# Performance work log

Measured on AMD Instinct MI355X. Metric: run time of the kernel, lower is better.

## Reference

```python
import jax, jax.numpy as jnp
import numpy as np

D, F, E, K = 1024, 2048, 8, 2
EPS = 1.1920929e-07  # torch.finfo(float32).eps, RMSNorm default eps=None


def setup_inputs() -> dict:
    key = jax.random.key(0)
    ks = jax.random.split(key, 6)
    x = jax.random.normal(ks[0], (2, 2048, D), jnp.float32)
    Wg = jax.random.normal(ks[1], (D, E), jnp.float32)          # Gate.weights ~ randn
    norm_w = jnp.ones((E, D), jnp.float32)                       # per-expert RMSNorm weight
    W1 = jax.random.normal(ks[2], (E, D, F), jnp.float32) * 0.02
    b1 = jnp.zeros((E, F), jnp.float32)
    W2 = jax.random.normal(ks[3], (E, D, F), jnp.float32) * 0.02
    b2 = jnp.zeros((E, F), jnp.float32)
    W3 = jax.random.normal(ks[4], (E, F, D), jnp.float32) * 0.02
    b3 = jnp.zeros((E, D), jnp.float32)
    return {"x": x, "Wg": Wg, "norm_w": norm_w, "W1": W1, "b1": b1,
            "W2": W2, "b2": b2, "W3": W3, "b3": b3, "k": K}


def reference(x, Wg, norm_w, W1, b1, W2, b2, W3, b3, k):
    orig_shape = x.shape
    xt = x.reshape(-1, x.shape[-1])                    # [T, d]
    num_experts = Wg.shape[-1]

    # --- Gate: top-k then softmax over selected logits ---
    scores = xt @ Wg                                   # [T, E]
    top_v, top_i = jax.lax.top_k(scores, k)            # [T, k]
    gates = jax.nn.softmax(top_v, axis=-1)             # [T, k]
    # combine weight per (token, expert); zero for unrouted experts
    comb = jnp.einsum('tk,tke->te', gates,
                      jax.nn.one_hot(top_i, num_experts, dtype=gates.dtype))  # [T, E]

    # --- Per-expert SwiGLU FFN with RMSNorm (norm weight folded into W1/W2) ---
    inv = jax.lax.rsqrt(jnp.mean(xt * xt, axis=-1, keepdims=True) + EPS)
    xh = xt * inv                                      # [T, d] (un-weighted RMSNorm)
    W1p = norm_w[:, :, None] * W1                      # [E, d, f]
    W2p = norm_w[:, :, None] * W2
    a = jnp.einsum('td,edf->etf', xh, W1p) + b1[:, None, :]   # [E, T, f]
    g = jnp.einsum('td,edf->etf', xh, W2p) + b2[:, None, :]
    h = jax.nn.silu(a) * g                             # [E, T, f]
    o = jnp.einsum('etf,efd->etd', h, W3) + b3[:, None, :]    # [E, T, d]

    # --- Weighted combine (comb==0 for unrouted -> identical to masked loop) ---
    y = jnp.einsum('etd,te->td', o, comb)              # [T, d]
    return y.reshape(orig_shape)
```

## Files before the change

### kernel.cpp

```cpp
#include <hip/hip_runtime.h>
#include <hip/hip_bf16.h>

typedef unsigned short u16;
typedef __attribute__((ext_vector_type(8))) short bf16x8;
typedef __attribute__((ext_vector_type(4))) float f32x4;

#define D_DIM 1024
#define F_DIM 2048
#define E_NUM 8
#define EPS_RMS 1.1920929e-07f
#define NCHUNK 16

__device__ __forceinline__ u16 f2bf(float f) {
  union { float f; unsigned u; } v; v.f = f;
  unsigned r = v.u + 0x7FFFu + ((v.u >> 16) & 1u);
  return (u16)(r >> 16);
}

__device__ __forceinline__ void async16(const void* g, void* l) {
  __builtin_amdgcn_global_load_lds((const __attribute__((address_space(1))) void*)g,
                                   (__attribute__((address_space(3))) void*)l, 16, 0, 0);
}

__global__ __launch_bounds__(256) void prep_kernel(
    const float* __restrict__ W1, const float* __restrict__ W2,
    const float* __restrict__ W3, const float* __restrict__ scale,
    const float* __restrict__ x, const float* __restrict__ Wg,
    u16* __restrict__ Wc, u16* __restrict__ W3t, u16* __restrict__ xh,
    int* __restrict__ topi, float* __restrict__ gatev)
{
  __shared__ float tile[128][65];
  __shared__ float red[4][9];
  __shared__ float invs;
  const int lin = blockIdx.x;
  const int tid = threadIdx.x;

  if (lin < 4096) {
    const int z = lin >> 8;
    const int rem = lin & 255;
    const int fb = (rem & 31) * 64;
    const int db = (rem >> 5) * 128;
    const int e = z & 7;
    const float* W = (z < 8) ? W1 : W2;
    const int gofs = (z < 8) ? 0 : 16;
    const float* Wp = W + (size_t)e * D_DIM * F_DIM;
#pragma unroll
    for (int s = 0; s < 8; ++s) {
      const int d = (tid >> 4) + s * 16;
      float4 v = *reinterpret_cast<const float4*>(Wp + (size_t)(db + d) * F_DIM + fb + (tid & 15) * 4);
      tile[d][(tid&15)*4+0] = v.x; tile[d][(tid&15)*4+1] = v.y;
      tile[d][(tid&15)*4+2] = v.z; tile[d][(tid&15)*4+3] = v.w;
    }
    __syncthreads();
    const int dx = (tid & 31) * 4;
    float sc[4];
#pragma unroll
    for (int q = 0; q < 4; ++q) sc[q] = scale[(size_t)e * D_DIM + db + dx + q];
    u16* op = Wc + (size_t)e * (2*F_DIM) * D_DIM;
#pragma unroll
    for (int p = 0; p < 8; ++p) {
      const int j = (tid >> 5) + p * 8;
      const int c = fb + j;
      const int rphys = ((c >> 4) << 5) + (c & 15) + gofs;
      u16 tmp[4];
#pragma unroll
      for (int q = 0; q < 4; ++q) tmp[q] = f2bf(tile[dx + q][j] * sc[q]);
      *reinterpret_cast<ushort4*>(op + (size_t)rphys * D_DIM + db + dx) =
          *reinterpret_cast<ushort4*>(tmp);
    }
  } else if (lin < 6144) {
    const int l2 = lin - 4096;
    const int e = l2 >> 8;
    const int rem = l2 & 255;
    const int dt = (rem & 15) * 64;
    const int ft = (rem >> 4) * 128;
    const float* Wp = W3 + (size_t)e * F_DIM * D_DIM;
#pragma unroll
    for (int s = 0; s < 8; ++s) {
      const int fr = (tid >> 4) + s * 16;
      float4 v = *reinterpret_cast<const float4*>(Wp + (size_t)(ft + fr) * D_DIM + dt + (tid & 15) * 4);
      tile[fr][(tid&15)*4+0] = v.x; tile[fr][(tid&15)*4+1] = v.y;
      tile[fr][(tid&15)*4+2] = v.z; tile[fr][(tid&15)*4+3] = v.w;
    }
    __syncthreads();
    const int fx = (tid & 31) * 4;
    u16* op = W3t + (size_t)e * D_DIM * F_DIM;
#pragma unroll
    for (int p = 0; p < 8; ++p) {
      const int j = (tid >> 5) + p * 8;
      u16 tmp[4];
#pragma unroll
      for (int q = 0; q < 4; ++q) tmp[q] = f2bf(tile[fx + q][j]);
      *reinterpret_cast<ushort4*>(op + (size_t)(dt + j) * F_DIM + ft + fx) =
          *reinterpret_cast<ushort4*>(tmp);
    }
  } else {
    const int t = lin - 6144;
    const float4 xv = reinterpret_cast<const float4*>(x + (size_t)t * D_DIM)[tid];
    float ss = xv.x*xv.x + xv.y*xv.y + xv.z*xv.z + xv.w*xv.w;
    float s[8];
#pragma unroll
    for (int e = 0; e < 8; ++e) s[e] = 0.f;
    const float xa[4] = {xv.x, xv.y, xv.z, xv.w};
#pragma unroll
    for (int j = 0; j < 4; ++j) {
      const float4* wr = reinterpret_cast<const float4*>(Wg + (size_t)(tid*4 + j) * 8);
      float4 w0 = wr[0], w1 = wr[1];
      s[0] += xa[j]*w0.x; s[1] += xa[j]*w0.y; s[2] += xa[j]*w0.z; s[3] += xa[j]*w0.w;
      s[4] += xa[j]*w1.x; s[5] += xa[j]*w1.y; s[6] += xa[j]*w1.z; s[7] += xa[j]*w1.w;
    }
#pragma unroll
    for (int off = 32; off > 0; off >>= 1) {
      ss += __shfl_down(ss, off);
#pragma unroll
      for (int e = 0; e < 8; ++e) s[e] += __shfl_down(s[e], off);
    }
    const int wv = tid >> 6, lane = tid & 63;
    if (lane == 0) { red[wv][8] = ss;
#pragma unroll
      for (int e = 0; e < 8; ++e) red[wv][e] = s[e]; }
    __syncthreads();
    if (tid == 0) {
      float sum2 = red[0][8] + red[1][8] + red[2][8] + red[3][8];
      invs = rsqrtf(sum2 * (1.0f / D_DIM) + EPS_RMS);
      float sc[8];
#pragma unroll
      for (int e = 0; e < 8; ++e) sc[e] = red[0][e] + red[1][e] + red[2][e] + red[3][e];
      int i0 = 0; float v0 = sc[0];
#pragma unroll
      for (int e = 1; e < 8; ++e) if (sc[e] > v0) { v0 = sc[e]; i0 = e; }
      int i1 = -1; float v1 = -3.0e38f;
#pragma unroll
      for (int e = 0; e < 8; ++e) if (e != i0 && sc[e] > v1) { v1 = sc[e]; i1 = e; }
      float p1 = 1.0f / (1.0f + expf(v0 - v1));
      float p0 = 1.0f - p1;
      topi[2*t] = i0; topi[2*t+1] = i1;
      gatev[2*t] = p0; gatev[2*t+1] = p1;
    }
    __syncthreads();
    const float inv = invs;
    ushort4 o;
    o.x = f2bf(xv.x*inv); o.y = f2bf(xv.y*inv); o.z = f2bf(xv.z*inv); o.w = f2bf(xv.w*inv);
    reinterpret_cast<ushort4*>(xh + (size_t)t * D_DIM)[tid] = o;
  }
}

__global__ __launch_bounds__(256) void count_kernel(
    const int* __restrict__ topi, int* __restrict__ percnt, int nent)
{
  const int blk = blockIdx.x;
  const int tid = threadIdx.x;
  const int per = (nent + NCHUNK*256 - 1) / (NCHUNK*256);
  const int cbase = blk * 256 * per;
  int c[8];
#pragma unroll
  for (int q = 0; q < 8; ++q) c[q] = 0;
  for (int i = 0; i < per; ++i) {
    const int idx = cbase + tid * per + i;
    if (idx < nent) {
      const int e = topi[idx];
#pragma unroll
      for (int q = 0; q < 8; ++q) c[q] += (e == q) ? 1 : 0;
    }
  }
#pragma unroll
  for (int off = 32; off > 0; off >>= 1)
#pragma unroll
    for (int q = 0; q < 8; ++q) c[q] += __shfl_down(c[q], off);
  __shared__ int red[4][8];
  const int wv = tid >> 6, lane = tid & 63;
  if (lane == 0)
#pragma unroll
    for (int q = 0; q < 8; ++q) red[wv][q] = c[q];
  __syncthreads();
  if (tid < 8) percnt[blk * 8 + tid] = red[0][tid] + red[1][tid] + red[2][tid] + red[3][tid];
}

__global__ __launch_bounds__(256) void scatter_kernel(
    const int* __restrict__ topi, const int* __restrict__ percnt,
    int* __restrict__ rowtok, int* __restrict__ slots, int* __restrict__ offs, int nent)
{
  __shared__ int cur[8];
  const int blk = blockIdx.x, tid = threadIdx.x;
  if (tid == 0) {
    int tot[8];
#pragma unroll
    for (int e = 0; e < 8; ++e) {
      tot[e] = 0;
      for (int c = 0; c < NCHUNK; ++c) tot[e] += percnt[c*8 + e];
    }
    int acc = 0, start[8];
#pragma unroll
    for (int e = 0; e < 8; ++e) {
      start[e] = acc;
      if (blk == 0) offs[e] = acc;
      acc += (tot[e] + 255) & ~255;
    }
    if (blk == 0) offs[8] = acc;
    for (int c = 0; c < blk; ++c)
#pragma unroll
      for (int e = 0; e < 8; ++e) start[e] += percnt[c*8 + e];
#pragma unroll
    for (int e = 0; e < 8; ++e) cur[e] = start[e];
  }
  __syncthreads();
  const int per = (nent + NCHUNK*256 - 1) / (NCHUNK*256);
  const int cbase = blk * 256 * per;
  for (int i = 0; i < per; ++i) {
    const int idx = cbase + tid * per + i;
    if (idx < nent) {
      const int e = topi[idx];
      const int pos = atomicAdd(&cur[e], 1);
      rowtok[pos] = idx >> 1;
      slots[idx] = pos;
    }
  }
}

__global__ __launch_bounds__(512, 4) void ffn1_kernel(
    const u16* __restrict__ xh, const u16* __restrict__ Wc,
    const float* __restrict__ b1, const float* __restrict__ b2,
    const int* __restrict__ rowtok, const int* __restrict__ offs,
    u16* __restrict__ h)
{
  __shared__ __align__(16) u16 smem[36864];

  const int row0 = blockIdx.y * 256;
  if (row0 >= offs[8]) return;
  int e = 0;
#pragma unroll
  for (int i = 1; i < 8; ++i) e += (row0 >= offs[i]) ? 1 : 0;

  const int bx = blockIdx.x;
  const int n0p = bx * 128;
  const int tid = threadIdx.x;
  const int lane = tid & 63;
  const int l15 = lane & 15;
  const int wv = tid >> 6;
  const int wm = wv >> 1;
  const int wn = wv & 1;

  int arow[2];
  const u16* gAp[2];
#pragma unroll
  for (int j = 0; j < 2; ++j) {
    const int i = tid + 512*j;
    const int p = i >> 3;
    const int v = (i & 7) ^ (p & 7);
    arow[j] = 2*p + (v >> 2);
    int tk = rowtok[row0 + arow[j]];
    if (tk < 0) tk = 0;
    gAp[j] = xh + (size_t)tk * D_DIM + (v & 3) * 8;
  }
  const u16* gBp;
  {
    const int i = tid;
    const int p = i >> 3;
    const int v = (i & 7) ^ (p & 7);
    const int brow = 2*p + (v >> 2);
    gBp = Wc + ((size_t)e * (2*F_DIM) + n0p + brow) * D_DIM + (v & 3) * 8;
  }

  const f32x4 zero = {0.f, 0.f, 0.f, 0.f};
  f32x4 acc[4][4];
#pragma unroll
  for (int i = 0; i < 4; ++i)
#pragma unroll
    for (int j = 0; j < 4; ++j) acc[i][j] = zero;

  const int rlane = (((l15 & 1) << 2) + (lane >> 4)) ^ (l15 >> 1);
  const int aoff = (l15 >> 1) * 64 + rlane * 8;
  const int boff = (l15 >> 1) * 64 + rlane * 8;

#define STAGE1(b, k0)                                                       \
  {                                                                         \
    const int base_ = (b) * 12288;                                          \
    async16(gAp[0] + (k0), &smem[base_ + tid*8]);                           \
    async16(gAp[1] + (k0), &smem[base_ + (tid + 512)*8]);                   \
    async16(gBp   + (k0), &smem[base_ + 8192 + tid*8]);                     \
  }

  STAGE1(0, 0);
  STAGE1(1, 32);

  const int NSTEP = D_DIM / 32;
  for (int t = 0; t < NSTEP; ++t) {
    const int bsel = t % 3;
    if (t + 1 < NSTEP) {
      asm volatile("s_waitcnt vmcnt(3)" ::: "memory");
    } else {
      asm volatile("s_waitcnt vmcnt(0)" ::: "memory");
    }
    __builtin_amdgcn_s_barrier();
    if (t + 2 < NSTEP) {
      const int bn = (t + 2) % 3;
      const int kn = (t + 2) * 32;
      STAGE1(bn, kn);
    }
    const int aB = bsel * 12288, bB = aB + 8192;
    bf16x8 af[4], bv[4];
#pragma unroll
    for (int mi = 0; mi < 4; ++mi)
      af[mi] = *(const bf16x8*)(&smem[aB + (wm*32 + mi*8)*64 + aoff]);
#pragma unroll
    for (int ni = 0; ni < 4; ++ni)
      bv[ni] = *(const bf16x8*)(&smem[bB + (wn*32 + ni*8)*64 + boff]);
#pragma unroll
    for (int mi = 0; mi < 4; ++mi)
#pragma unroll
      for (int ni = 0; ni < 4; ++ni)
        acc[mi][ni] = __builtin_amdgcn_mfma_f32_16x16x32_bf16(af[mi], bv[ni], acc[mi][ni], 0, 0, 0);
  }
#undef STAGE1

#pragma unroll
  for (int mi = 0; mi < 4; ++mi) {
    const int rbase = row0 + wm*64 + mi*16 + (lane >> 4)*4;
#pragma unroll
    for (int q = 0; q < 2; ++q) {
      const int rc = bx*64 + wn*32 + q*16 + l15;
      const float bb1 = b1[e*F_DIM + rc], bb2 = b2[e*F_DIM + rc];
#pragma unroll
      for (int r = 0; r < 4; ++r) {
        float a = acc[mi][2*q][r] + bb1;
        float g = acc[mi][2*q+1][r] + bb2;
        h[(size_t)(rbase + r) * F_DIM + rc] = f2bf(a / (1.f + __expf(-a)) * g);
      }
    }
  }
}

__global__ __launch_bounds__(256, 2) void ffn2_kernel(
    const u16* __restrict__ h, const u16* __restrict__ W3t,
    const float* __restrict__ b3, const int* __restrict__ offs,
    float* __restrict__ opart)
{
  __shared__ __align__(16) u16 smem[32768];

  const int lin = blockIdx.y * gridDim.x + blockIdx.x;
  const int qc  = (gridDim.x * gridDim.y) >> 3;
  const int L   = (lin & 7) * qc + (lin >> 3);
  const int bx  = L % gridDim.x;
  const int by  = L / gridDim.x;

  const int row0 = by * 128;
  if (row0 >= offs[8]) return;
  int e = 0;
#pragma unroll
  for (int i = 1; i < 8; ++i) e += (row0 >= offs[i]) ? 1 : 0;

  const int n0 = bx * 128;
  const int tid = threadIdx.x;
  const int lane = tid & 63;
  const int wv = tid >> 6;
  const int wm = wv >> 1;
  const int wn = wv & 1;

  const int srow = tid >> 3;
  const int sseg = (tid & 7) ^ (srow & 7);
  const u16* gA[4]; const u16* gB[4];
#pragma unroll
  for (int j = 0; j < 4; ++j) {
    gA[j] = h   + (size_t)(row0 + srow + 32*j) * F_DIM + sseg * 8;
    gB[j] = W3t + ((size_t)e * D_DIM + n0 + srow + 32*j) * F_DIM + sseg * 8;
  }

  const f32x4 zero = {0.f, 0.f, 0.f, 0.f};
  f32x4 acc[4][4];
#pragma unroll
  for (int i = 0; i < 4; ++i)
#pragma unroll
    for (int j = 0; j < 4; ++j) acc[i][j] = zero;

  const int rswz = (lane & 7) << 3;
  const int kpart = (lane >> 4) * 8;
  const int arowbase = (wm*64 + (lane & 15)) * 64;
  const int browbase = (wn*64 + (lane & 15)) * 64;

#define STAGE2(b, k0)                                                       \
  {                                                                         \
    const int aB_ = (b)*8192, bB_ = 16384 + (b)*8192;                       \
    _Pragma("unroll")                                                       \
    for (int j = 0; j < 4; ++j) {                                           \
      async16(gA[j] + (k0), &smem[aB_ + (tid + 256*j)*8]);                  \
      async16(gB[j] + (k0), &smem[bB_ + (tid + 256*j)*8]);                  \
    }                                                                       \
  }

  STAGE2(0, 0);
  __syncthreads();

  int cur = 0;
  for (int t = 0; t < F_DIM/64; ++t) {
    if (t + 1 < F_DIM/64) STAGE2(cur ^ 1, (t+1)*64);
    const int aB = cur*8192, bB = 16384 + cur*8192;
#pragma unroll
    for (int kk = 0; kk < 2; ++kk) {
      const int ko = kk*32 + kpart;
      bf16x8 af[4], bv[4];
#pragma unroll
      for (int mi = 0; mi < 4; ++mi)
        af[mi] = *(const bf16x8*)(&smem[aB + ((arowbase + mi*1024 + ko) ^ rswz)]);
#pragma unroll
      for (int ni = 0; ni < 4; ++ni)
        bv[ni] = *(const bf16x8*)(&smem[bB + ((browbase + ni*1024 + ko) ^ rswz)]);
#pragma unroll
      for (int mi = 0; mi < 4; ++mi)
#pragma unroll
        for (int ni = 0; ni < 4; ++ni)
          acc[mi][ni] = __builtin_amdgcn_mfma_f32_16x16x32_bf16(af[mi], bv[ni], acc[mi][ni], 0, 0, 0);
    }
    __syncthreads();
    cur ^= 1;
  }
#undef STAGE2

#pragma unroll
  for (int mi = 0; mi < 4; ++mi) {
    const int rbase = row0 + wm*64 + mi*16 + (lane >> 4)*4;
#pragma unroll
    for (int ni = 0; ni < 4; ++ni) {
      const int gc = n0 + wn*64 + ni*16 + (lane & 15);
      const float bb = b3[e*D_DIM + gc];
#pragma unroll
      for (int r = 0; r < 4; ++r)
        opart[(size_t)(rbase + r) * D_DIM + gc] = acc[mi][ni][r] + bb;
    }
  }
}

__global__ __launch_bounds__(256) void combine_kernel(
    const float* __restrict__ opart, const int* __restrict__ slots,
    const float* __restrict__ gatev, float* __restrict__ y)
{
  const int t = blockIdx.x;
  const int s0 = slots[2*t], s1 = slots[2*t+1];
  const float w0 = gatev[2*t], w1 = gatev[2*t+1];
  const float4 a = reinterpret_cast<const float4*>(opart + (size_t)s0 * D_DIM)[threadIdx.x];
  const float4 b = reinterpret_cast<const float4*>(opart + (size_t)s1 * D_DIM)[threadIdx.x];
  float4 o;
  o.x = w0*a.x + w1*b.x; o.y = w0*a.y + w1*b.y;
  o.z = w0*a.z + w1*b.z; o.w = w0*a.w + w1*b.w;
  reinterpret_cast<float4*>(y + (size_t)t * D_DIM)[threadIdx.x] = o;
}

extern "C" void kernel_launch(void* const* d_in, const int* in_sizes, int n_in,
                              void* d_out, int out_size, void* d_ws, size_t ws_size,
                              hipStream_t stream)
{
  const float* x  = (const float*)d_in[0];
  const float* Wg = (const float*)d_in[1];
  const float* nw = (const float*)d_in[2];
  const float* W1 = (const float*)d_in[3];
  const float* b1 = (const float*)d_in[4];
  const float* W2 = (const float*)d_in[5];
  const float* b2 = (const float*)d_in[6];
  const float* W3 = (const float*)d_in[7];
  const float* b3 = (const float*)d_in[8];
  float* y = (float*)d_out;

  const int T = in_sizes[0] / D_DIM;
  const int NENT = T * 2;
  const int RCAP = ((NENT + E_NUM * 255) + 255) & ~255;
  const int MT1 = RCAP / 256;
  const int MT2 = RCAP / 128;

  char* ws = (char*)d_ws;
  size_t off_ = 0;
  auto take = [&](size_t bytes) { char* p = ws + off_; off_ = (off_ + bytes + 255) & ~(size_t)255; return p; };
  u16* Wc     = (u16*)take((size_t)E_NUM * 2 * F_DIM * D_DIM * 2);
  u16* W3t    = (u16*)take((size_t)E_NUM * D_DIM * F_DIM * 2);
  u16* xh     = (u16*)take((size_t)T * D_DIM * 2);
  u16* hbuf   = (u16*)take((size_t)RCAP * F_DIM * 2);
  int* rowtok = (int*)take((size_t)RCAP * 4);
  int* slots  = (int*)take((size_t)NENT * 4);
  int* topi   = (int*)take((size_t)NENT * 4);
  float* gatev= (float*)take((size_t)NENT * 4);
  int* percnt = (int*)take(NCHUNK * 8 * 4);
  int* offs   = (int*)take(64);
  float* opart = (float*)Wc;
  (void)ws_size; (void)n_in; (void)out_size;

  (void)hipMemsetAsync(rowtok, 0xFF, (size_t)RCAP * 4, stream);

  prep_kernel<<<6144 + T, 256, 0, stream>>>(W1, W2, W3, nw, x, Wg, Wc, W3t, xh, topi, gatev);
  count_kernel<<<NCHUNK, 256, 0, stream>>>(topi, percnt, NENT);
  scatter_kernel<<<NCHUNK, 256, 0, stream>>>(topi, percnt, rowtok, slots, offs, NENT);

  ffn1_kernel<<<dim3((2*F_DIM)/128, MT1), 512, 0, stream>>>(xh, Wc, b1, b2, rowtok, offs, hbuf);
  ffn2_kernel<<<dim3(D_DIM/128, MT2), 256, 0, stream>>>(hbuf, W3t, b3, offs, opart);
  combine_kernel<<<T, 256, 0, stream>>>(opart, slots, gatev, y);
}
```

Measured before the change: 234.5 us.

## Restructure weight prep transpose to bf16 LDS tiles with full-row wide stores

```diff
diff --git a/kernel.cpp b/kernel.cpp
--- a/kernel.cpp
+++ b/kernel.cpp
@@ -22,89 +22,86 @@
                                    (__attribute__((address_space(3))) void*)l, 16, 0, 0);
 }
 
-__global__ __launch_bounds__(256) void prep_kernel(
+__global__ __launch_bounds__(512) void prep_kernel(
     const float* __restrict__ W1, const float* __restrict__ W2,
     const float* __restrict__ W3, const float* __restrict__ scale,
     const float* __restrict__ x, const float* __restrict__ Wg,
     u16* __restrict__ Wc, u16* __restrict__ W3t, u16* __restrict__ xh,
     int* __restrict__ topi, float* __restrict__ gatev)
 {
-  __shared__ float tile[128][65];
-  __shared__ float red[4][9];
+  __shared__ u16 lbuf[32][1026];
+  __shared__ float red[8][9];
   __shared__ float invs;
   const int lin = blockIdx.x;
   const int tid = threadIdx.x;
 
-  if (lin < 4096) {
-    const int z = lin >> 8;
-    const int rem = lin & 255;
-    const int fb = (rem & 31) * 64;
-    const int db = (rem >> 5) * 128;
+  if (lin < 1024) {
+    const int z = lin >> 6;
+    const int fb = (lin & 63) * 32;
     const int e = z & 7;
     const float* W = (z < 8) ? W1 : W2;
     const int gofs = (z < 8) ? 0 : 16;
     const float* Wp = W + (size_t)e * D_DIM * F_DIM;
-#pragma unroll
-    for (int s = 0; s < 8; ++s) {
-      const int d = (tid >> 4) + s * 16;
-      float4 v = *reinterpret_cast<const float4*>(Wp + (size_t)(db + d) * F_DIM + fb + (tid & 15) * 4);
-      tile[d][(tid&15)*4+0] = v.x; tile[d][(tid&15)*4+1] = v.y;
-      tile[d][(tid&15)*4+2] = v.z; tile[d][(tid&15)*4+3] = v.w;
+    const int fq = tid & 7;
+#pragma unroll
+    for (int it = 0; it < 16; ++it) {
+      const int d = it * 64 + (tid >> 3);
+      const float4 v = *reinterpret_cast<const float4*>(Wp + (size_t)d * F_DIM + fb + fq * 4);
+      const float s = scale[(size_t)e * D_DIM + d];
+      lbuf[fq*4+0][d] = f2bf(v.x * s);
+      lbuf[fq*4+1][d] = f2bf(v.y * s);
+      lbuf[fq*4+2][d] = f2bf(v.z * s);
+      lbuf[fq*4+3][d] = f2bf(v.w * s);
     }
     __syncthreads();
-    const int dx = (tid & 31) * 4;
-    float sc[4];
-#pragma unroll
-    for (int q = 0; q < 4; ++q) sc[q] = scale[(size_t)e * D_DIM + db + dx + q];
     u16* op = Wc + (size_t)e * (2*F_DIM) * D_DIM;
 #pragma unroll
-    for (int p = 0; p < 8; ++p) {
-      const int j = (tid >> 5) + p * 8;
-      const int c = fb + j;
-      const int rphys = ((c >> 4) << 5) + (c & 15) + gofs;
-      u16 tmp[4];
-#pragma unroll
-      for (int q = 0; q < 4; ++q) tmp[q] = f2bf(tile[dx + q][j] * sc[q]);
-      *reinterpret_cast<ushort4*>(op + (size_t)rphys * D_DIM + db + dx) =
-          *reinterpret_cast<ushort4*>(tmp);
-    }
-  } else if (lin < 6144) {
-    const int l2 = lin - 4096;
-    const int e = l2 >> 8;
-    const int rem = l2 & 255;
-    const int dt = (rem & 15) * 64;
-    const int ft = (rem >> 4) * 128;
+    for (int it = 0; it < 8; ++it) {
+      const int idx = it * 512 + tid;
+      const int r = idx >> 7;
+      const int c = idx & 127;
+      const int rphys = ((fb + r) >> 4) * 32 + (r & 15) + gofs;
+      *reinterpret_cast<int4*>(op + (size_t)rphys * D_DIM + c * 8) =
+          *reinterpret_cast<const int4*>(&lbuf[r][c * 8]);
+    }
+  } else if (lin < 1536) {
+    const int l2 = lin - 1024;
+    const int e = l2 >> 6;
+    const int rem = l2 & 63;
+    const int db = (rem >> 1) * 32;
+    const int fhb = (rem & 1) * 1024;
     const float* Wp = W3 + (size_t)e * F_DIM * D_DIM;
-#pragma unroll
-    for (int s = 0; s < 8; ++s) {
-      const int fr = (tid >> 4) + s * 16;
-      float4 v = *reinterpret_cast<const float4*>(Wp + (size_t)(ft + fr) * D_DIM + dt + (tid & 15) * 4);
-      tile[fr][(tid&15)*4+0] = v.x; tile[fr][(tid&15)*4+1] = v.y;
-      tile[fr][(tid&15)*4+2] = v.z; tile[fr][(tid&15)*4+3] = v.w;
+    const int dq = tid & 7;
+#pragma unroll
+    for (int it = 0; it < 16; ++it) {
+      const int f = it * 64 + (tid >> 3);
+      const float4 v = *reinterpret_cast<const float4*>(Wp + (size_t)(fhb + f) * D_DIM + db + dq * 4);
+      lbuf[dq*4+0][f] = f2bf(v.x);
+      lbuf[dq*4+1][f] = f2bf(v.y);
+      lbuf[dq*4+2][f] = f2bf(v.z);
+      lbuf[dq*4+3][f] = f2bf(v.w);
     }
     __syncthreads();
-    const int fx = (tid & 31) * 4;
     u16* op = W3t + (size_t)e * D_DIM * F_DIM;
 #pragma unroll
-    for (int p = 0; p < 8; ++p) {
-      const int j = (tid >> 5) + p * 8;
-      u16 tmp[4];
-#pragma unroll
-      for (int q = 0; q < 4; ++q) tmp[q] = f2bf(tile[fx + q][j]);
-      *reinterpret_cast<ushort4*>(op + (size_t)(dt + j) * F_DIM + ft + fx) =
-          *reinterpret_cast<ushort4*>(tmp);
+    for (int it = 0; it < 8; ++it) {
+      const int idx = it * 512 + tid;
+      const int r = idx >> 7;
+      const int c = idx & 127;
+      *reinterpret_cast<int4*>(op + (size_t)(db + r) * F_DIM + fhb + c * 8) =
+          *reinterpret_cast<const int4*>(&lbuf[r][c * 8]);
     }
   } else {
-    const int t = lin - 6144;
-    const float4 xv = reinterpret_cast<const float4*>(x + (size_t)t * D_DIM)[tid];
-    float ss = xv.x*xv.x + xv.y*xv.y + xv.z*xv.z + xv.w*xv.w;
+    const int t = lin - 1536;
+    const float2 xv = reinterpret_cast<const float2*>(x + (size_t)t * D_DIM)[tid];
+    float ss = xv.x*xv.x + xv.y*xv.y;
     float s[8];
 #pragma unroll
     for (int e = 0; e < 8; ++e) s[e] = 0.f;
-    const float xa[4] = {xv.x, xv.y, xv.z, xv.w};
-#pragma unroll
-    for (int j = 0; j < 4; ++j) {
-      const float4* wr = reinterpret_cast<const float4*>(Wg + (size_t)(tid*4 + j) * 8);
+    const float xa[2] = {xv.x, xv.y};
+#pragma unroll
+    for (int j = 0; j < 2; ++j) {
+      const float4* wr = reinterpret_cast<const float4*>(Wg + (size_t)(tid*2 + j) * 8);
       float4 w0 = wr[0], w1 = wr[1];
       s[0] += xa[j]*w0.x; s[1] += xa[j]*w0.y; s[2] += xa[j]*w0.z; s[3] += xa[j]*w0.w;
       s[4] += xa[j]*w1.x; s[5] += xa[j]*w1.y; s[6] += xa[j]*w1.z; s[7] += xa[j]*w1.w;
@@ -121,11 +118,17 @@
       for (int e = 0; e < 8; ++e) red[wv][e] = s[e]; }
     __syncthreads();
     if (tid == 0) {
-      float sum2 = red[0][8] + red[1][8] + red[2][8] + red[3][8];
+      float sum2 = 0.f;
+#pragma unroll
+      for (int w = 0; w < 8; ++w) sum2 += red[w][8];
       invs = rsqrtf(sum2 * (1.0f / D_DIM) + EPS_RMS);
       float sc[8];
 #pragma unroll
-      for (int e = 0; e < 8; ++e) sc[e] = red[0][e] + red[1][e] + red[2][e] + red[3][e];
+      for (int e = 0; e < 8; ++e) {
+        sc[e] = 0.f;
+#pragma unroll
+        for (int w = 0; w < 8; ++w) sc[e] += red[w][e];
+      }
       int i0 = 0; float v0 = sc[0];
 #pragma unroll
       for (int e = 1; e < 8; ++e) if (sc[e] > v0) { v0 = sc[e]; i0 = e; }
@@ -139,9 +142,9 @@
     }
     __syncthreads();
     const float inv = invs;
-    ushort4 o;
-    o.x = f2bf(xv.x*inv); o.y = f2bf(xv.y*inv); o.z = f2bf(xv.z*inv); o.w = f2bf(xv.w*inv);
-    reinterpret_cast<ushort4*>(xh + (size_t)t * D_DIM)[tid] = o;
+    ushort2 o;
+    o.x = f2bf(xv.x*inv); o.y = f2bf(xv.y*inv);
+    reinterpret_cast<ushort2*>(xh + (size_t)t * D_DIM)[tid] = o;
   }
 }
 
@@ -483,7 +486,7 @@
 
   (void)hipMemsetAsync(rowtok, 0xFF, (size_t)RCAP * 4, stream);
 
-  prep_kernel<<<6144 + T, 256, 0, stream>>>(W1, W2, W3, nw, x, Wg, Wc, W3t, xh, topi, gatev);
+  prep_kernel<<<1536 + T, 512, 0, stream>>>(W1, W2, W3, nw, x, Wg, Wc, W3t, xh, topi, gatev);
   count_kernel<<<NCHUNK, 256, 0, stream>>>(topi, percnt, NENT);
   scatter_kernel<<<NCHUNK, 256, 0, stream>>>(topi, percnt, rowtok, slots, offs, NENT);
 
```

New measurement: 247.2 us. 1.05x slower.
